# Kernel optimization log

Measured on AMD Instinct MI355X. Metric: run time of the kernel, lower is better.

Reference implementation:

```python
import jax, jax.numpy as jnp
import numpy as np

B, P, K = 8, 4096, 16
NUM_CLASSES = 10


def _knn_idx(pos):
    # pos: [B,P,3] -> neighbor indices [B,P,K] (k nearest, excluding self)
    p = jax.lax.stop_gradient(pos)
    sq = jnp.sum(p * p, axis=-1)                      # [B,P]
    d2 = sq[:, :, None] + sq[:, None, :] - 2.0 * jnp.einsum('bpd,bqd->bpq', p, p)
    d2 = d2 + jnp.eye(P, dtype=p.dtype) * 1e10        # loop=False: mask self
    _, idx = jax.lax.top_k(-d2, K)                    # [B,P,K]
    return idx


def _tconv(x, idx, wq, bq, wk, bk, wv, bv, ws, bs):
    # PyG TransformerConv (heads=1, root_weight=True): x [B,P,din] -> [B,P,dout]
    d = wq.shape[1]
    q = x @ wq + bq                                   # [B,P,d]
    k = x @ wk + bk
    v = x @ wv + bv
    b_ix = jnp.arange(x.shape[0])[:, None, None]
    k_n = k[b_ix, idx]                                # [B,P,K,d] gather neighbor keys
    v_n = v[b_ix, idx]                                # [B,P,K,d]
    logits = jnp.einsum('bpd,bpkd->bpk', q, k_n) / jnp.sqrt(jnp.asarray(d, x.dtype))
    a = jax.nn.softmax(logits, axis=-1)               # softmax over the K neighbors (per target node)
    out = jnp.einsum('bpk,bpkd->bpd', a, v_n)
    return out + (x @ ws + bs)                        # skip connection


def setup_inputs() -> dict:
    key = jax.random.key(0)
    ks = jax.random.split(key, 32)
    inp = {'pos': jax.random.normal(ks[0], (B, P, 3), dtype=jnp.float32)}
    dims = [(3, 64), (64, 128), (128, 256)]
    i = 1
    for l, (din, dout) in enumerate(dims, start=1):
        s = 1.0 / np.sqrt(din)
        for nm in ('q', 'k', 'v', 's'):
            inp[f'w{l}{nm}'] = jax.random.normal(ks[i], (din, dout), dtype=jnp.float32) * s
            inp[f'b{l}{nm}'] = jnp.zeros((dout,), dtype=jnp.float32)
            i += 1
    for nm, (din, dout) in [('fc1', (256, 512)), ('fc2', (512, 256)), ('fc3', (256, NUM_CLASSES))]:
        inp[f'{nm}_w'] = jax.random.normal(ks[i], (din, dout), dtype=jnp.float32) / np.sqrt(din)
        inp[f'{nm}_b'] = jnp.zeros((dout,), dtype=jnp.float32)
        i += 1
    return inp


def reference(pos,
              w1q, b1q, w1k, b1k, w1v, b1v, w1s, b1s,
              w2q, b2q, w2k, b2k, w2v, b2v, w2s, b2s,
              w3q, b3q, w3k, b3k, w3v, b3v, w3s, b3s,
              fc1_w, fc1_b, fc2_w, fc2_b, fc3_w, fc3_b):
    idx = _knn_idx(pos)
    x = jax.nn.relu(_tconv(pos, idx, w1q, b1q, w1k, b1k, w1v, b1v, w1s, b1s))
    x = jax.nn.relu(_tconv(x, idx, w2q, b2q, w2k, b2k, w2v, b2v, w2s, b2s))
    x = jax.nn.relu(_tconv(x, idx, w3q, b3q, w3k, b3k, w3v, b3v, w3s, b3s))
    g = jnp.max(x, axis=1)                            # global_max_pool over points -> [B,256]
    g = jax.nn.relu(g @ fc1_w + fc1_b)                # dropout is identity at eval
    g = jax.nn.relu(g @ fc2_w + fc2_b)
    g = g @ fc3_w + fc3_b
    return jax.nn.log_softmax(g, axis=1)
```

## Files before the change

### kernel.cpp

```cpp
#include <hip/hip_runtime.h>
#include <math.h>

#define BATCH 8
#define NPTS  4096
#define NBR   16
#define MTOT  (BATCH * NPTS)

#define KNN_BINS  2048
#define KNN_SHIFT 21
#define KNN_PAD   (KNN_BINS + KNN_BINS / 32)
#define HADDR(b)  ((b) + ((b) >> 5))
#define KNN_CAP   384

typedef unsigned short ushort_t;
typedef __attribute__((ext_vector_type(8))) short bf16x8;
typedef __attribute__((ext_vector_type(4))) float f32x4;

__device__ inline unsigned short f2bf(float f) {
  unsigned u = __float_as_uint(f);
  return (unsigned short)((u + 0x7FFFu + ((u >> 16) & 1u)) >> 16);
}
__device__ inline float bff(unsigned short h) {
  return __uint_as_float(((unsigned)h) << 16);
}
__device__ inline float2 bf2(unsigned u) {
  return make_float2(__uint_as_float(u << 16), __uint_as_float(u & 0xFFFF0000u));
}

__global__ __launch_bounds__(256) void prep_pos4(const float* __restrict__ pos,
                                                 float4* __restrict__ pos4) {
  int i = blockIdx.x * 256 + threadIdx.x;
  float x = pos[i * 3 + 0], y = pos[i * 3 + 1], z = pos[i * 3 + 2];
  pos4[i] = make_float4(x, y, z, x * x + y * y + z * z);
}

__global__ __launch_bounds__(256) void knn_kernel(const float4* __restrict__ pos4,
                                                  int* __restrict__ idxout,
                                                  int tbase) {
  __shared__ __align__(16) unsigned hist[KNN_PAD];
  __shared__ unsigned wsum[4];
  __shared__ unsigned long long cand[KNN_CAP];
  __shared__ unsigned nC, s_bmin;

  int t = tbase + blockIdx.x;
  int b = t >> 12;
  int p = t & (NPTS - 1);
  const float4* base = pos4 + ((size_t)b << 12);
  float4 me = base[p];

  int tid = threadIdx.x;
  int lane = tid & 63, wv = tid >> 6;
#pragma unroll
  for (int i = 0; i < 3; ++i) {
    int w = tid + i * 256;
    if (w < KNN_PAD / 4) ((uint4*)hist)[w] = make_uint4(0u, 0u, 0u, 0u);
  }
  if (tid == 0) nC = 0;
  __syncthreads();

  unsigned key[16];
  unsigned mn = 0xFFFFFFFFu;
#pragma unroll
  for (int j = 0; j < 16; ++j) {
    int q = tid + j * 256;
    float4 o = base[q];
    float dx = me.x - o.x, dy = me.y - o.y, dz = me.z - o.z;
    float d2 = dx * dx + dy * dy + dz * dz;
    unsigned k = __float_as_uint(d2);
    key[j] = (q == p) ? 0xFFFFFFFFu : k;
    mn = (key[j] < mn) ? key[j] : mn;
  }
  atomicAdd(&hist[HADDR(mn >> KNN_SHIFT)], 1u);
  __syncthreads();

  unsigned s = 0;
#pragma unroll
  for (int i = 0; i < 8; ++i) s += hist[HADDR(tid * 8 + i)];
  unsigned c = s;
#pragma unroll
  for (int d = 1; d < 64; d <<= 1) {
    unsigned x = __shfl_up(c, d);
    if (lane >= d) c += x;
  }
  if (lane == 63) wsum[wv] = c;
  __syncthreads();
  unsigned off = 0;
#pragma unroll
  for (int w = 0; w < 4; ++w) off += (w < wv) ? wsum[w] : 0u;
  unsigned cum_incl = c + off;
  unsigned cum_excl = cum_incl - s;

  if (cum_excl < NBR && cum_incl >= NBR) {
    unsigned h[8];
#pragma unroll
    for (int i = 0; i < 8; ++i) h[i] = hist[HADDR(tid * 8 + i)];
    unsigned c0 = cum_excl; int bin = tid * 8; bool done = false;
#pragma unroll
    for (int i = 0; i < 8; ++i) {
      if (!done) {
        if (c0 + h[i] >= NBR) done = true;
        else { c0 += h[i]; ++bin; }
      }
    }
    s_bmin = (unsigned)bin;
  }
  __syncthreads();
  unsigned kmax = (s_bmin << KNN_SHIFT) | ((1u << KNN_SHIFT) - 1u);

#pragma unroll
  for (int j = 0; j < 16; ++j) {
    if (key[j] <= kmax) {
      int q = tid + j * 256;
      float4 o = base[q];
      float d2r = me.w + o.w - 2.f * (me.x * o.x + me.y * o.y + me.z * o.z);
      unsigned u = __float_as_uint(d2r);
      unsigned fk = u ^ (unsigned)(((int)u >> 31) | 0x80000000);
      unsigned slot = atomicAdd(&nC, 1u);
      if (slot < KNN_CAP)
        cand[slot] = ((unsigned long long)fk << 32) | (unsigned)q;
    }
  }
  __syncthreads();

  int n = (int)(nC < KNN_CAP ? nC : KNN_CAP);
  int* op = idxout + (size_t)t * NBR;
  for (int sidx = tid; sidx < n; sidx += 256) {
    unsigned long long my = cand[sidx];
    int cnt = 0;
    for (int r = 0; r < n; ++r) cnt += (cand[r] < my) ? 1 : 0;
    if (cnt < NBR) op[cnt] = (int)(my & 0xFFFFFFFFu);
  }
}

__global__ void l1_pre(const float* __restrict__ wq, const float* __restrict__ bq,
                       const float* __restrict__ wk, const float* __restrict__ bk,
                       float* __restrict__ l1c) {
  int t = threadIdx.x;
  if (t < 9) {
    int a = t / 3, b = t % 3;
    float s = 0.f;
    for (int c = 0; c < 64; ++c) s += wq[a * 64 + c] * wk[b * 64 + c];
    l1c[t] = s;
  } else if (t < 12) {
    int a = t - 9;
    float s = 0.f;
    for (int c = 0; c < 64; ++c) s += wq[a * 64 + c] * bk[c];
    l1c[t] = s;
  } else if (t < 15) {
    int b = t - 12;
    float s = 0.f;
    for (int c = 0; c < 64; ++c) s += wk[b * 64 + c] * bq[c];
    l1c[t] = s;
  } else if (t == 15) {
    float s = 0.f;
    for (int c = 0; c < 64; ++c) s += bq[c] * bk[c];
    l1c[t] = s;
  }
}

__global__ __launch_bounds__(256) void l1_fused(const float4* __restrict__ pos4,
    const int* __restrict__ idx, const float* __restrict__ l1c,
    const float* __restrict__ wvw, const float* __restrict__ bv,
    const float* __restrict__ wsw, const float* __restrict__ bs,
    ushort_t* __restrict__ xsh, ushort_t* __restrict__ xsl) {
  __shared__ float wvs[192], wss[192], bcs[64], cc[16];
  __shared__ float4 pts[16];
  __shared__ int ss[256];
  int tid = threadIdx.x;
  int t0 = blockIdx.x * 16;
  int bofs = (t0 >> 12) << 12;
  if (tid < 192) wvs[tid] = wvw[tid];
  if (tid >= 64) wss[tid - 64] = wsw[tid - 64];
  if (tid < 64) bcs[tid] = bv[tid] + bs[tid];
  if (tid < 16) pts[tid] = pos4[t0 + tid];
  else if (tid >= 16 && tid < 32) cc[tid - 16] = l1c[tid - 16];
  ss[tid] = bofs + idx[t0 * 16 + tid];
  __syncthreads();
  int lane = tid & 63, wq = tid >> 6;
  int tt = lane >> 4, jj = lane & 15;
  int tgt = wq * 4 + tt;
  float4 pj = pos4[ss[tid]];
  float4 pt = pts[tgt];
  float r0 = cc[0] * pj.x + cc[1] * pj.y + cc[2] * pj.z;
  float r1 = cc[3] * pj.x + cc[4] * pj.y + cc[5] * pj.z;
  float r2 = cc[6] * pj.x + cc[7] * pj.y + cc[8] * pj.z;
  float logit = pt.x * (r0 + cc[9]) + pt.y * (r1 + cc[10]) + pt.z * (r2 + cc[11])
              + cc[12] * pj.x + cc[13] * pj.y + cc[14] * pj.z + cc[15];
  logit *= 0.125f;
  float mx = logit;
#pragma unroll
  for (int d = 1; d <= 8; d <<= 1) mx = fmaxf(mx, __shfl_xor(mx, d));
  float e = expf(logit - mx);
  float sm = e;
#pragma unroll
  for (int d = 1; d <= 8; d <<= 1) sm += __shfl_xor(sm, d);
  float a = e / sm;
  float ax = a * pj.x, ay = a * pj.y, az = a * pj.z;
#pragma unroll
  for (int d = 1; d <= 8; d <<= 1) {
    ax += __shfl_xor(ax, d);
    ay += __shfl_xor(ay, d);
    az += __shfl_xor(az, d);
  }
  ushort4 h, l;
  float v0, v1, v2, v3;
  {
    int c = 4 * jj;
    v0 = ax * wvs[c + 0] + ay * wvs[64 + c + 0] + az * wvs[128 + c + 0]
       + pt.x * wss[c + 0] + pt.y * wss[64 + c + 0] + pt.z * wss[128 + c + 0] + bcs[c + 0];
    v1 = ax * wvs[c + 1] + ay * wvs[64 + c + 1] + az * wvs[128 + c + 1]
       + pt.x * wss[c + 1] + pt.y * wss[64 + c + 1] + pt.z * wss[128 + c + 1] + bcs[c + 1];
    v2 = ax * wvs[c + 2] + ay * wvs[64 + c + 2] + az * wvs[128 + c + 2]
       + pt.x * wss[c + 2] + pt.y * wss[64 + c + 2] + pt.z * wss[128 + c + 2] + bcs[c + 2];
    v3 = ax * wvs[c + 3] + ay * wvs[64 + c + 3] + az * wvs[128 + c + 3]
       + pt.x * wss[c + 3] + pt.y * wss[64 + c + 3] + pt.z * wss[128 + c + 3] + bcs[c + 3];
  }
  v0 = fmaxf(v0, 0.f); v1 = fmaxf(v1, 0.f);
  v2 = fmaxf(v2, 0.f); v3 = fmaxf(v3, 0.f);
  h.x = f2bf(v0); l.x = f2bf(v0 - bff(h.x));
  h.y = f2bf(v1); l.y = f2bf(v1 - bff(h.y));
  h.z = f2bf(v2); l.z = f2bf(v2 - bff(h.z));
  h.w = f2bf(v3); l.w = f2bf(v3 - bff(h.w));
  size_t ofs = (size_t)(t0 + tgt) * 64 + 4 * jj;
  *(ushort4*)(xsh + ofs) = h;
  *(ushort4*)(xsl + ofs) = l;
}

template <int K, int SECN>
__global__ __launch_bounds__(256) void split_wt4(const float* __restrict__ w0,
    const float* __restrict__ w1, const float* __restrict__ w2,
    const float* __restrict__ w3,
    ushort_t* __restrict__ th, ushort_t* __restrict__ tl) {
  int i = blockIdx.x * 256 + threadIdx.x;
  if (i >= 4 * K * SECN) return;
  int nm = i / (K * SECN);
  int w = i - nm * (K * SECN);
  int k = w / SECN, n = w - k * SECN;
  const float* wp = (nm == 0) ? w0 : (nm == 1) ? w1 : (nm == 2) ? w2 : w3;
  float v = wp[w];
  unsigned short hh = f2bf(v);
  size_t dst = (size_t)(nm * SECN + n) * K + k;
  th[dst] = hh;
  tl[dst] = f2bf(v - bff(hh));
}

template <int K, int SECN>
__global__ __launch_bounds__(256) void gemm4(const ushort_t* __restrict__ Xh,
    const ushort_t* __restrict__ Xl,
    const ushort_t* __restrict__ Wth, const ushort_t* __restrict__ Wtl,
    const float* __restrict__ bq, const float* __restrict__ bk,
    const float* __restrict__ bv, const float* __restrict__ bs,
    ushort_t* __restrict__ qout, ushort_t* __restrict__ kout,
    ushort_t* __restrict__ vout, float* __restrict__ sout) {
  __shared__ __align__(16) ushort_t cst[4][32 * 72];
  int lane = threadIdx.x & 63, wv = threadIdx.x >> 6;
  int bm = blockIdx.x * 128 + (wv >> 1) * 64;
  int gn = blockIdx.y * 128 + (wv & 1) * 64;
  int r = lane & 15, g4 = lane >> 4;
  f32x4 acc[4][4];
#pragma unroll
  for (int i = 0; i < 4; ++i)
#pragma unroll
    for (int j = 0; j < 4; ++j) acc[i][j] = (f32x4){0.f, 0.f, 0.f, 0.f};

  for (int k0 = 0; k0 < K; k0 += 32) {
    int kb = k0 + g4 * 8;
    bf16x8 ah[4], al[4], bh[4], bl[4];
#pragma unroll
    for (int i = 0; i < 4; ++i) {
      size_t xo = (size_t)(bm + i * 16 + r) * K + kb;
      ah[i] = *(const bf16x8*)(Xh + xo);
      al[i] = *(const bf16x8*)(Xl + xo);
      size_t wo = (size_t)(gn + i * 16 + r) * K + kb;
      bh[i] = *(const bf16x8*)(Wth + wo);
      bl[i] = *(const bf16x8*)(Wtl + wo);
    }
#pragma unroll
    for (int i = 0; i < 4; ++i)
#pragma unroll
      for (int j = 0; j < 4; ++j) {
        acc[i][j] = __builtin_amdgcn_mfma_f32_16x16x32_bf16(ah[i], bh[j], acc[i][j], 0, 0, 0);
        acc[i][j] = __builtin_amdgcn_mfma_f32_16x16x32_bf16(ah[i], bl[j], acc[i][j], 0, 0, 0);
        acc[i][j] = __builtin_amdgcn_mfma_f32_16x16x32_bf16(al[i], bh[j], acc[i][j], 0, 0, 0);
      }
  }
  int sec = gn / SECN;
  int colbase = gn - sec * SECN;
  const float* bp = (sec == 0) ? bq : (sec == 1) ? bk : (sec == 2) ? bv : bs;
  if (sec == 3) {
#pragma unroll
    for (int j = 0; j < 4; ++j) {
      int col = colbase + j * 16 + r;
      float bias = bp[col];
#pragma unroll
      for (int i = 0; i < 4; ++i)
#pragma unroll
        for (int tr = 0; tr < 4; ++tr) {
          int row = bm + i * 16 + g4 * 4 + tr;
          sout[(size_t)row * SECN + col] = acc[i][j][tr] + bias;
        }
    }
  } else {
    ushort_t* outp = (sec == 0) ? qout : (sec == 1) ? kout : vout;
    ushort_t* cw = cst[wv];
#pragma unroll
    for (int half = 0; half < 2; ++half) {
#pragma unroll
      for (int j = 0; j < 4; ++j) {
        int col = j * 16 + r;
        float bias = bp[colbase + col];
#pragma unroll
        for (int i = 0; i < 2; ++i)
#pragma unroll
          for (int tr = 0; tr < 4; ++tr)
            cw[(i * 16 + g4 * 4 + tr) * 72 + col] =
                f2bf(acc[2 * half + i][j][tr] + bias);
      }
#pragma unroll
      for (int it = 0; it < 4; ++it) {
        int row = (lane >> 3) + it * 8;
        int cs = (lane & 7) * 8;
        uint4 v4 = *(uint4*)&cw[row * 72 + cs];
        *(uint4*)&outp[(size_t)(bm + half * 32 + row) * SECN + colbase + cs] = v4;
      }
    }
  }
}

template <int DOUT, bool OUTSPLIT>
__global__ __launch_bounds__(256) void attn_kernel(const ushort_t* __restrict__ qp,
                                                   const ushort_t* __restrict__ kp,
                                                   const ushort_t* __restrict__ vp,
                                                   const int* __restrict__ idx,
                                                   const float* xin,
                                                   void* outa,
                                                   ushort_t* outl,
                                                   float* pbuf) {
  constexpr int F   = DOUT / 4;
  constexpr int CPL = DOUT / 16;
  __shared__ float4 qs[4][4][F + 1];
  __shared__ int    ss[4][64];
  int lane = threadIdx.x & 63, wv = threadIdx.x >> 6;
  int swz = (blockIdx.x & 7) * (MTOT / 16 / 8) + (blockIdx.x >> 3);
  int t0 = swz * 16 + wv * 4;
  int bofs = (t0 >> 12) << 12;
  int tt = lane >> 4, jj = lane & 15;
  int src = bofs + idx[(t0 + tt) * 16 + jj];
  ss[wv][lane] = src;
  const uint4* qp4 = (const uint4*)(qp + (size_t)t0 * DOUT);
#pragma unroll
  for (int i = 0; i < DOUT / 128; ++i) {
    int g = lane + 64 * i;
    uint4 qv = qp4[g];
    int row = g / (DOUT / 8), e8 = g % (DOUT / 8);
    float2 a0 = bf2(qv.x), a1 = bf2(qv.y), a2 = bf2(qv.z), a3 = bf2(qv.w);
    qs[wv][row][2 * e8]     = make_float4(a0.x, a0.y, a1.x, a1.y);
    qs[wv][row][2 * e8 + 1] = make_float4(a2.x, a2.y, a3.x, a3.y);
  }
  __syncthreads();

  const uint4* krow = (const uint4*)(kp + (size_t)src * DOUT);
  float acc = 0.f;
#pragma unroll
  for (int cch = 0; cch < DOUT / 8; ++cch) {
    uint4 kk = krow[cch];
    float4 q0 = qs[wv][tt][2 * cch], q1 = qs[wv][tt][2 * cch + 1];
    float2 k0 = bf2(kk.x), k1 = bf2(kk.y), k2 = bf2(kk.z), k3 = bf2(kk.w);
    acc += q0.x * k0.x + q0.y * k0.y + q0.z * k1.x + q0.w * k1.y
         + q1.x * k2.x + q1.y * k2.y + q1.z * k3.x + q1.w * k3.y;
  }
  const float scale = (DOUT == 128) ? 0.08838834764831843f : 0.0625f;
  float logit = acc * scale;
  float mx = logit;
#pragma unroll
  for (int d = 1; d <= 8; d <<= 1) mx = fmaxf(mx, __shfl_xor(mx, d));
  float e = expf(logit - mx);
  float sm = e;
#pragma unroll
  for (int d = 1; d <= 8; d <<= 1) sm += __shfl_xor(sm, d);
  float a = e / sm;

  float4 o[CPL / 4];
#pragma unroll
  for (int c = 0; c < CPL / 4; ++c) o[c] = make_float4(0.f, 0.f, 0.f, 0.f);
  int gbase = lane & 48;
#pragma unroll
  for (int j = 0; j < 16; ++j) {
    float aj = __shfl(a, gbase | j);
    const ushort_t* vr = vp + (size_t)ss[wv][gbase | j] * DOUT + CPL * jj;
#pragma unroll
    for (int c = 0; c < CPL / 8; ++c) {
      uint4 vv = ((const uint4*)vr)[c];
      float2 a0 = bf2(vv.x), a1 = bf2(vv.y), a2 = bf2(vv.z), a3 = bf2(vv.w);
      o[2 * c].x += aj * a0.x;     o[2 * c].y += aj * a0.y;
      o[2 * c].z += aj * a1.x;     o[2 * c].w += aj * a1.y;
      o[2 * c + 1].x += aj * a2.x; o[2 * c + 1].y += aj * a2.y;
      o[2 * c + 1].z += aj * a3.x; o[2 * c + 1].w += aj * a3.y;
    }
  }

  size_t chbase = (size_t)(t0 + tt) * DOUT + CPL * jj;
  const float4* xi4 = (const float4*)(xin + chbase);
  float4 rr[CPL / 4];
#pragma unroll
  for (int c = 0; c < CPL / 4; ++c) {
    float4 x4 = xi4[c];
    rr[c].x = fmaxf(x4.x + o[c].x, 0.f);
    rr[c].y = fmaxf(x4.y + o[c].y, 0.f);
    rr[c].z = fmaxf(x4.z + o[c].z, 0.f);
    rr[c].w = fmaxf(x4.w + o[c].w, 0.f);
  }
  if constexpr (OUTSPLIT) {
#pragma unroll
    for (int c = 0; c < CPL / 4; ++c) {
      ushort4 h, l;
      h.x = f2bf(rr[c].x); l.x = f2bf(rr[c].x - bff(h.x));
      h.y = f2bf(rr[c].y); l.y = f2bf(rr[c].y - bff(h.y));
      h.z = f2bf(rr[c].z); l.z = f2bf(rr[c].z - bff(h.z));
      h.w = f2bf(rr[c].w); l.w = f2bf(rr[c].w - bff(h.w));
      *(ushort4*)((ushort_t*)outa + chbase + 4 * c) = h;
      *(ushort4*)(outl + chbase + 4 * c) = l;
    }
  } else {
#pragma unroll
    for (int c = 0; c < CPL / 4; ++c) {
#pragma unroll
      for (int mask = 16; mask <= 32; mask <<= 1) {
        rr[c].x = fmaxf(rr[c].x, __shfl_xor(rr[c].x, mask));
        rr[c].y = fmaxf(rr[c].y, __shfl_xor(rr[c].y, mask));
        rr[c].z = fmaxf(rr[c].z, __shfl_xor(rr[c].z, mask));
        rr[c].w = fmaxf(rr[c].w, __shfl_xor(rr[c].w, mask));
      }
    }
    if (lane < 16) {
      float4* pb = (float4*)(pbuf + ((size_t)(swz * 4 + wv) * 256) + CPL * jj);
#pragma unroll
      for (int c = 0; c < CPL / 4; ++c) pb[c] = rr[c];
    }
  }
}

__global__ void zero_kernel(float* g) { g[blockIdx.x * 256 + threadIdx.x] = 0.f; }

__global__ __launch_bounds__(256) void pool_reduce(const float* __restrict__ pbuf,
                                                   float* __restrict__ g) {
  int b = blockIdx.y, s = blockIdx.x, ch = threadIdx.x;
  const float* base = pbuf + ((size_t)b * 1024 + s * 128) * 256 + ch;
  float m = 0.f;
  for (int w = 0; w < 128; ++w) m = fmaxf(m, base[w * 256]);
  atomicMax((int*)&g[b * 256 + ch], __float_as_int(m));
}

__global__ __launch_bounds__(256) void head_kernel(const float* __restrict__ g,
    const float* __restrict__ w1, const float* __restrict__ b1,
    const float* __restrict__ w2, const float* __restrict__ b2,
    const float* __restrict__ w3, const float* __restrict__ b3,
    float* __restrict__ out) {
  __shared__ float gb[256], h1[512], h2[256], lg[10];
  int b = blockIdx.x, t = threadIdx.x;
  gb[t] = g[b * 256 + t];
  __syncthreads();
#pragma unroll
  for (int half = 0; half < 2; ++half) {
    int c = t + half * 256;
    float a = b1[c];
    for (int kk = 0; kk < 256; ++kk) a += gb[kk] * w1[kk * 512 + c];
    h1[c] = fmaxf(a, 0.f);
  }
  __syncthreads();
  {
    float a = b2[t];
    for (int kk = 0; kk < 512; ++kk) a += h1[kk] * w2[kk * 256 + t];
    h2[t] = fmaxf(a, 0.f);
  }
  __syncthreads();
  if (t < 10) {
    float a = b3[t];
    for (int kk = 0; kk < 256; ++kk) a += h2[kk] * w3[kk * 10 + t];
    lg[t] = a;
  }
  __syncthreads();
  if (t < 10) {
    float mx = lg[0];
#pragma unroll
    for (int i = 1; i < 10; ++i) mx = fmaxf(mx, lg[i]);
    float s = 0.f;
#pragma unroll
    for (int i = 0; i < 10; ++i) s += expf(lg[i] - mx);
    out[b * 10 + t] = lg[t] - mx - logf(s);
  }
}

extern "C" void kernel_launch(void* const* d_in, const int* in_sizes, int n_in,
                              void* d_out, int out_size, void* d_ws, size_t ws_size,
                              hipStream_t stream) {
  const float* pos = (const float*)d_in[0];
  const float* W[3][4]; const float* Bb[3][4];
  for (int l = 0; l < 3; ++l)
    for (int nm = 0; nm < 4; ++nm) {
      W[l][nm]  = (const float*)d_in[1 + l * 8 + nm * 2];
      Bb[l][nm] = (const float*)d_in[1 + l * 8 + nm * 2 + 1];
    }
  const float* fc1w = (const float*)d_in[25]; const float* fc1b = (const float*)d_in[26];
  const float* fc2w = (const float*)d_in[27]; const float* fc2b = (const float*)d_in[28];
  const float* fc3w = (const float*)d_in[29]; const float* fc3b = (const float*)d_in[30];

  int*   idxb  = (int*)d_ws;
  float* fbase = (float*)((char*)d_ws + (size_t)MTOT * NBR * 4);
  float* qb = fbase;
  float* kb = qb + (size_t)MTOT * 256;
  float* vb = kb + (size_t)MTOT * 256;
  float* x2 = vb + (size_t)MTOT * 256;
  float* x3 = x2 + (size_t)MTOT * 128;
  float* g  = x3 + (size_t)MTOT * 256;
  float4* pos4 = (float4*)(g + BATCH * 256);
  ushort_t* xsh = (ushort_t*)(pos4 + MTOT);
  ushort_t* xsl = xsh + (size_t)MTOT * 128;
  ushort_t* th2 = xsl + (size_t)MTOT * 128;
  ushort_t* tl2 = th2 + 512 * 64;
  ushort_t* th3 = tl2 + 512 * 64;
  ushort_t* tl3 = th3 + 1024 * 128;
  float*    l1c = (float*)(tl3 + 1024 * 128);
  float*    pbuf = l1c + 64;
  ushort_t* qh = (ushort_t*)qb;
  ushort_t* kh = (ushort_t*)kb;
  ushort_t* vh = (ushort_t*)vb;

  prep_pos4<<<MTOT / 256, 256, 0, stream>>>(pos, pos4);
  knn_kernel<<<MTOT / 2, 256, 0, stream>>>(pos4, idxb, 0);
  knn_kernel<<<MTOT / 2, 256, 0, stream>>>(pos4, idxb, MTOT / 2);

  l1_pre<<<1, 64, 0, stream>>>(W[0][0], Bb[0][0], W[0][1], Bb[0][1], l1c);
  l1_fused<<<MTOT / 16, 256, 0, stream>>>(pos4, idxb, l1c,
                                          W[0][2], Bb[0][2], W[0][3], Bb[0][3],
                                          xsh, xsl);

  split_wt4<64, 128><<<(4 * 64 * 128 + 255) / 256, 256, 0, stream>>>(
      W[1][0], W[1][1], W[1][2], W[1][3], th2, tl2);
  gemm4<64, 128><<<dim3(MTOT / 128, 4), 256, 0, stream>>>(
      xsh, xsl, th2, tl2, Bb[1][0], Bb[1][1], Bb[1][2], Bb[1][3],
      qh, kh, vh, x2);
  attn_kernel<128, true><<<MTOT / 16, 256, 0, stream>>>(qh, kh, vh, idxb, x2,
                                                        xsh, xsl, nullptr);

  split_wt4<128, 256><<<(4 * 128 * 256 + 255) / 256, 256, 0, stream>>>(
      W[2][0], W[2][1], W[2][2], W[2][3], th3, tl3);
  gemm4<128, 256><<<dim3(MTOT / 128, 8), 256, 0, stream>>>(
      xsh, xsl, th3, tl3, Bb[2][0], Bb[2][1], Bb[2][2], Bb[2][3],
      qh, kh, vh, x3);
  attn_kernel<256, false><<<MTOT / 16, 256, 0, stream>>>(qh, kh, vh, idxb, x3,
                                                         nullptr, nullptr, pbuf);

  zero_kernel<<<8, 256, 0, stream>>>(g);
  pool_reduce<<<dim3(8, 8), 256, 0, stream>>>(pbuf, g);
  head_kernel<<<8, 256, 0, stream>>>(g, fc1w, fc1b, fc2w, fc2b, fc3w, fc3b,
                                     (float*)d_out);
}
```

Measured before the change: 364.3 us.

## Stage GEMM operand tiles in shared memory for reuse across waves

The projection GEMM now cooperatively loads the hi/lo bf16 X and W tiles for each K-step into LDS, one wave per operand, and every wave then reads its fragments from LDS. Before, each wave loaded its own fragments straight from global memory, so each tile was fetched twice per block. The change halves redundant global traffic but adds two block barriers per K-step and no double buffering, so load latency is no longer overlapped with MFMA work. The epilogue staging buffer now reuses the same LDS array.

```diff
diff --git a/kernel.cpp b/kernel.cpp
--- a/kernel.cpp
+++ b/kernel.cpp
@@ -252,10 +252,13 @@
     const float* __restrict__ bv, const float* __restrict__ bs,
     ushort_t* __restrict__ qout, ushort_t* __restrict__ kout,
     ushort_t* __restrict__ vout, float* __restrict__ sout) {
-  __shared__ __align__(16) ushort_t cst[4][32 * 72];
+  __shared__ __align__(16) ushort_t tile[4][128 * 40];
   int lane = threadIdx.x & 63, wv = threadIdx.x >> 6;
-  int bm = blockIdx.x * 128 + (wv >> 1) * 64;
-  int gn = blockIdx.y * 128 + (wv & 1) * 64;
+  int bm0 = blockIdx.x * 128;
+  int gn0 = blockIdx.y * 128;
+  int wm = wv >> 1, wn = wv & 1;
+  int bm = bm0 + wm * 64;
+  int gn = gn0 + wn * 64;
   int r = lane & 15, g4 = lane >> 4;
   f32x4 acc[4][4];
 #pragma unroll
@@ -263,17 +266,29 @@
 #pragma unroll
     for (int j = 0; j < 4; ++j) acc[i][j] = (f32x4){0.f, 0.f, 0.f, 0.f};
 
+  const ushort_t* sp = (wv == 0) ? Xh : (wv == 1) ? Xl : (wv == 2) ? Wth : Wtl;
+  int rbase = (wv < 2) ? bm0 : gn0;
+  ushort_t* dst = tile[wv];
+  int srow = lane >> 2;
+  int skof = (lane & 3) * 8;
+
   for (int k0 = 0; k0 < K; k0 += 32) {
-    int kb = k0 + g4 * 8;
+#pragma unroll
+    for (int p = 0; p < 8; ++p) {
+      int row = p * 16 + srow;
+      uint4 v = *(const uint4*)(sp + (size_t)(rbase + row) * K + k0 + skof);
+      *(uint4*)&dst[row * 40 + skof] = v;
+    }
+    __syncthreads();
     bf16x8 ah[4], al[4], bh[4], bl[4];
 #pragma unroll
     for (int i = 0; i < 4; ++i) {
-      size_t xo = (size_t)(bm + i * 16 + r) * K + kb;
-      ah[i] = *(const bf16x8*)(Xh + xo);
-      al[i] = *(const bf16x8*)(Xl + xo);
-      size_t wo = (size_t)(gn + i * 16 + r) * K + kb;
-      bh[i] = *(const bf16x8*)(Wth + wo);
-      bl[i] = *(const bf16x8*)(Wtl + wo);
+      int ra = (wm * 64 + i * 16 + r) * 40 + g4 * 8;
+      int rb = (wn * 64 + i * 16 + r) * 40 + g4 * 8;
+      ah[i] = *(const bf16x8*)&tile[0][ra];
+      al[i] = *(const bf16x8*)&tile[1][ra];
+      bh[i] = *(const bf16x8*)&tile[2][rb];
+      bl[i] = *(const bf16x8*)&tile[3][rb];
     }
 #pragma unroll
     for (int i = 0; i < 4; ++i)
@@ -283,7 +298,9 @@
         acc[i][j] = __builtin_amdgcn_mfma_f32_16x16x32_bf16(ah[i], bl[j], acc[i][j], 0, 0, 0);
         acc[i][j] = __builtin_amdgcn_mfma_f32_16x16x32_bf16(al[i], bh[j], acc[i][j], 0, 0, 0);
       }
-  }
+    __syncthreads();
+  }
+
   int sec = gn / SECN;
   int colbase = gn - sec * SECN;
   const float* bp = (sec == 0) ? bq : (sec == 1) ? bk : (sec == 2) ? bv : bs;
@@ -302,7 +319,7 @@
     }
   } else {
     ushort_t* outp = (sec == 0) ? qout : (sec == 1) ? kout : vout;
-    ushort_t* cw = cst[wv];
+    ushort_t* cw = tile[wv];
 #pragma unroll
     for (int half = 0; half < 2; ++half) {
 #pragma unroll
```

After: 324.4 us. -11.0%, faster.
